# Performance work log

Hardware: AMD Instinct MI355X
Metric: run time of the kernel (lower is better)

The kernel has to match this reference:

```python
import jax, jax.numpy as jnp
import numpy as np

MIN_WEIGHT = 0.1
NEIGH = 2  # consistency_neigh
INV_LOG2 = 1.0 / np.log(2.0)


def _entropy_logits(y):
    # 1 + (p*(y - log(exp(y)+1)) - (1-p)*log(exp(y)+1)) / log(2)
    p = jax.nn.sigmoid(y)
    sp = jax.nn.softplus(y)  # log(exp(y) + 1)
    return 1.0 + (p * (y - sp) - (1.0 - p) * sp) * INV_LOG2


def _consistency(y):
    # 24-offset shifted-neighbor stencil: accumulate squared differences of
    # sigmoid probabilities against each in-bounds neighbor, normalize by the
    # per-pixel valid-neighbor count.
    probas = jax.nn.sigmoid(y)
    _, _, H, W = y.shape
    acc = jnp.zeros_like(y)
    div = jnp.zeros(y.shape, dtype=y.dtype)
    for off_x in range(-NEIGH, NEIGH + 1):
        for off_y in range(-NEIGH, NEIGH + 1):
            if off_x == 0 and off_y == 0:
                continue
            ryl, ryh = max(0, off_y), min(H, H + off_y)
            rxl, rxh = max(0, off_x), min(W, W + off_x)
            tyl, tyh = max(0, -off_y), min(H, H - off_y)
            txl, txh = max(0, -off_x), min(W, W - off_x)
            d = jnp.square(probas[:, :, ryl:ryh, rxl:rxh]
                           - probas[:, :, tyl:tyh, txl:txh])
            acc = acc.at[:, :, ryl:ryh, rxl:rxh].add(d)
            div = div.at[:, :, ryl:ryh, rxl:rxh].add(1.0)
    return 1.0 - acc / div


def setup_inputs() -> dict:
    key = jax.random.key(0)
    k1, k2 = jax.random.split(key)
    y_d = jax.random.normal(k1, (32, 1, 768, 768), dtype=jnp.float32)
    y_gt = jax.random.uniform(k2, (32, 1, 768, 768), dtype=jnp.float32)
    return {"y_d": y_d, "y_gt": y_gt}


def reference(y_d, y_gt):
    # mode = 'pred_merged': consistency * entropy
    w = _consistency(y_d) * _entropy_logits(y_d)
    w = jnp.maximum(w, y_gt)
    w = (1.0 - MIN_WEIGHT) * w + MIN_WEIGHT
    # do_rescale: divide by per-image spatial mean
    w = w / jnp.mean(w, axis=(2, 3), keepdims=True)
    return w
```

## Files before the change

kernel.cpp:

```cpp
#include <hip/hip_runtime.h>

#define IMG_H 768
#define IMG_W 768
#define N_IMG 32
#define TILE 64
#define HALO 2
#define LW 68
#define INV_LOG2 1.44269504088896340736f
#define TILES_X 12
#define TILES_PER_IMG 144
#define NTILES (N_IMG * TILES_PER_IMG)
#define GRID1 1536

__device__ __forceinline__ float fast_sigmoid(float y) {
    return 1.0f / (1.0f + __expf(-y));
}

__global__ __launch_bounds__(256) void wk_pass1(
    const float* __restrict__ y_d, const float* __restrict__ y_gt,
    float* __restrict__ out, float* __restrict__ sums)
{
    __shared__ float pbuf[LW * LW];
    __shared__ float red[4];

    const int tid = threadIdx.x;
    const int c0 = (tid & 15) << 2;
    const int rb = (tid >> 4) << 2;

    for (int it = 0; it < 3; ++it) {
        const int tile = blockIdx.x + it * GRID1;
        const int img = tile / TILES_PER_IMG;
        const int t   = tile - img * TILES_PER_IMG;
        const int ti  = t / TILES_X;
        const int tj  = t - ti * TILES_X;
        const int gi0 = ti * TILE, gj0 = tj * TILE;

        const size_t img_off = (size_t)img * IMG_H * IMG_W;
        const float* __restrict__ yimg = y_d + img_off;
        const float* __restrict__ gimg = y_gt + img_off;
        float* __restrict__ oimg = out + img_off;
        const int gj = gj0 + c0;

        if (it > 0) __syncthreads();

        float4 yv4[4];
#pragma unroll
        for (int r = 0; r < 4; ++r)
            yv4[r] = *reinterpret_cast<const float4*>(
                &yimg[(size_t)(gi0 + rb + r) * IMG_W + gj]);

        float4 pv4[4], ev4[4];
#pragma unroll
        for (int r = 0; r < 4; ++r) {
            float yy[4] = {yv4[r].x, yv4[r].y, yv4[r].z, yv4[r].w};
            float pp[4], ee[4];
#pragma unroll
            for (int u = 0; u < 4; ++u) {
                float y  = yy[u];
                float E  = __expf(-fabsf(y));
                float tt = 1.0f + E;
                float rr = __fdividef(1.0f, tt);
                float p  = (y >= 0.0f) ? rr : E * rr;
                float sp = fmaxf(y, 0.0f) + __logf(tt);
                pp[u] = p;
                ee[u] = fmaf(fmaf(p, y, -sp), INV_LOG2, 1.0f);
            }
            pv4[r] = make_float4(pp[0], pp[1], pp[2], pp[3]);
            ev4[r] = make_float4(ee[0], ee[1], ee[2], ee[3]);
            *reinterpret_cast<float4*>(
                &pbuf[(rb + HALO + r) * LW + (c0 + HALO)]) = pv4[r];
        }

        for (int idx = tid; idx < 528; idx += 256) {
            int pr, pc;
            if (idx < 272) {
                int rsel = idx / 68;
                pr = (rsel < 2) ? rsel : (64 + rsel);
                pc = idx - rsel * 68;
            } else {
                int k = idx - 272;
                pr = (k >> 2) + 2;
                int h = k & 3;
                pc = (h < 2) ? h : (64 + h);
            }
            int gi_ = gi0 - HALO + pr;
            int gj_ = gj0 - HALO + pc;
            float p = 0.f;
            if ((unsigned)gi_ < (unsigned)IMG_H && (unsigned)gj_ < (unsigned)IMG_W)
                p = fast_sigmoid(yimg[(size_t)gi_ * IMG_W + gj_]);
            pbuf[pr * LW + pc] = p;
        }
        __syncthreads();

        float cxv[4], rcp5[4];
#pragma unroll
        for (int c = 0; c < 4; ++c) {
            int g = gj + c;
            cxv[c] = (float)(min(g, HALO) + min(IMG_W - 1 - g, HALO) + 1);
            rcp5[c] = __fdividef(1.0f, fmaf(5.0f, cxv[c], -1.0f));
        }

        float V1[8], V2[8];
#pragma unroll
        for (int cc = 0; cc < 8; ++cc) { V1[cc] = 0.f; V2[cc] = 0.f; }
#pragma unroll
        for (int k = 0; k < 5; ++k) {
            const float* row = &pbuf[(rb + k) * LW + c0];
            float4 A = *reinterpret_cast<const float4*>(row);
            float4 B = *reinterpret_cast<const float4*>(row + 4);
            float a[8] = {A.x, A.y, A.z, A.w, B.x, B.y, B.z, B.w};
#pragma unroll
            for (int cc = 0; cc < 8; ++cc) {
                V1[cc] += a[cc];
                V2[cc] = fmaf(a[cc], a[cc], V2[cc]);
            }
        }

        float lsum = 0.0f;

#pragma unroll
        for (int r = 0; r < 4; ++r) {
            const int gi = gi0 + rb + r;

            float4 g4 = *reinterpret_cast<const float4*>(
                &gimg[(size_t)gi * IMG_W + gj]);

            float t01 = V1[0] + V1[1], t12 = V1[1] + V1[2], t23 = V1[2] + V1[3];
            float t34 = V1[3] + V1[4], t45 = V1[4] + V1[5], t56 = V1[5] + V1[6];
            float S1v[4] = { t01 + t23 + V1[4], t12 + t34 + V1[5],
                             t23 + t45 + V1[6], t34 + t56 + V1[7] };
            float u01 = V2[0] + V2[1], u12 = V2[1] + V2[2], u23 = V2[2] + V2[3];
            float u34 = V2[3] + V2[4], u45 = V2[4] + V2[5], u56 = V2[5] + V2[6];
            float S2v[4] = { u01 + u23 + V2[4], u12 + u34 + V2[5],
                             u23 + u45 + V2[6], u34 + u56 + V2[7] };

            float cy = (float)(min(gi, HALO) + min(IMG_H - 1 - gi, HALO) + 1);
            float rc[4];
            if (cy == 5.0f) {
#pragma unroll
                for (int c = 0; c < 4; ++c) rc[c] = rcp5[c];
            } else {
#pragma unroll
                for (int c = 0; c < 4; ++c)
                    rc[c] = __fdividef(1.0f, fmaf(cy, cxv[c], -1.0f));
            }

            float pcv[4] = {pv4[r].x, pv4[r].y, pv4[r].z, pv4[r].w};
            float ev[4]  = {ev4[r].x, ev4[r].y, ev4[r].z, ev4[r].w};
            float gv[4]  = {g4.x, g4.y, g4.z, g4.w};
            float wv[4];
#pragma unroll
            for (int c = 0; c < 4; ++c) {
                float pc = pcv[c];
                float C = cy * cxv[c];
                float acc = fmaf(C * pc, pc, fmaf(-2.0f * pc, S1v[c], S2v[c]));
                float cons = fmaf(-acc, rc[c], 1.0f);
                float w = fmaxf(cons * ev[c], gv[c]);
                w = fmaf(w, 0.9f, 0.1f);
                wv[c] = w;
                lsum += w;
            }
            *reinterpret_cast<float4*>(&oimg[(size_t)gi * IMG_W + gj]) =
                make_float4(wv[0], wv[1], wv[2], wv[3]);

            if (r < 3) {
                const float* rin  = &pbuf[(rb + r + 5) * LW + c0];
                const float* rout = &pbuf[(rb + r) * LW + c0];
                float4 IA = *reinterpret_cast<const float4*>(rin);
                float4 IB = *reinterpret_cast<const float4*>(rin + 4);
                float4 OA = *reinterpret_cast<const float4*>(rout);
                float4 OB = *reinterpret_cast<const float4*>(rout + 4);
                float vin[8]  = {IA.x, IA.y, IA.z, IA.w, IB.x, IB.y, IB.z, IB.w};
                float vout[8] = {OA.x, OA.y, OA.z, OA.w, OB.x, OB.y, OB.z, OB.w};
#pragma unroll
                for (int cc = 0; cc < 8; ++cc) {
                    V1[cc] += vin[cc] - vout[cc];
                    V2[cc] += fmaf(vin[cc], vin[cc], -(vout[cc] * vout[cc]));
                }
            }
        }

#pragma unroll
        for (int off = 32; off > 0; off >>= 1)
            lsum += __shfl_down(lsum, off, 64);
        if ((tid & 63) == 0) red[tid >> 6] = lsum;
        __syncthreads();
        if (tid == 0)
            atomicAdd(&sums[img], (red[0] + red[1]) + (red[2] + red[3]));
    }
}

__global__ __launch_bounds__(256) void wk_pass2(
    float* __restrict__ out, const float* __restrict__ sums)
{
    const size_t total4 = (size_t)N_IMG * IMG_H * IMG_W / 4;
    const int per_img4 = IMG_H * IMG_W / 4;
    for (size_t i = (size_t)blockIdx.x * blockDim.x + threadIdx.x; i < total4;
         i += (size_t)gridDim.x * blockDim.x) {
        int img = (int)(i / per_img4);
        float scale = (float)(IMG_H * IMG_W) / sums[img];
        float4 v = reinterpret_cast<float4*>(out)[i];
        v.x *= scale; v.y *= scale; v.z *= scale; v.w *= scale;
        reinterpret_cast<float4*>(out)[i] = v;
    }
}

extern "C" void kernel_launch(void* const* d_in, const int* in_sizes, int n_in,
                              void* d_out, int out_size, void* d_ws, size_t ws_size,
                              hipStream_t stream) {
    const float* y_d  = (const float*)d_in[0];
    const float* y_gt = (const float*)d_in[1];
    float* out  = (float*)d_out;
    float* sums = (float*)d_ws;

    hipMemsetAsync(sums, 0, N_IMG * sizeof(float), stream);

    wk_pass1<<<dim3(GRID1), dim3(256), 0, stream>>>(y_d, y_gt, out, sums);
    wk_pass2<<<dim3(2048), dim3(256), 0, stream>>>(out, sums);
}
```

Baseline: 94.75 us.

## Prefetch next tile's logits and issue halo/gt loads before compute

The persistent tile loop now loads the next tile's y_d values into registers during the current iteration. The halo values and the whole 4x4 block of y_gt are read before the sigmoid and entropy math rather than inside the output loop. This is meant to hide global-memory latency behind arithmetic and remove the extra barrier at the top of the loop. In exchange it holds more values in registers, which may lower occupancy.

```diff
diff --git a/kernel.cpp b/kernel.cpp
--- a/kernel.cpp
+++ b/kernel.cpp
@@ -27,69 +27,107 @@
     const int c0 = (tid & 15) << 2;
     const int rb = (tid >> 4) << 2;
 
+    int tile = blockIdx.x;
+    int img = tile / TILES_PER_IMG;
+    int tt  = tile - img * TILES_PER_IMG;
+    int ti  = tt / TILES_X;
+    int tj  = tt - ti * TILES_X;
+    int gi0 = ti * TILE, gj0 = tj * TILE;
+
+    float4 ycur[4];
+    {
+        const float* __restrict__ yimg = y_d + (size_t)img * IMG_H * IMG_W;
+#pragma unroll
+        for (int r = 0; r < 4; ++r)
+            ycur[r] = *reinterpret_cast<const float4*>(
+                &yimg[(size_t)(gi0 + rb + r) * IMG_W + gj0 + c0]);
+    }
+
     for (int it = 0; it < 3; ++it) {
-        const int tile = blockIdx.x + it * GRID1;
-        const int img = tile / TILES_PER_IMG;
-        const int t   = tile - img * TILES_PER_IMG;
-        const int ti  = t / TILES_X;
-        const int tj  = t - ti * TILES_X;
-        const int gi0 = ti * TILE, gj0 = tj * TILE;
-
         const size_t img_off = (size_t)img * IMG_H * IMG_W;
         const float* __restrict__ yimg = y_d + img_off;
         const float* __restrict__ gimg = y_gt + img_off;
         float* __restrict__ oimg = out + img_off;
         const int gj = gj0 + c0;
 
-        if (it > 0) __syncthreads();
-
-        float4 yv4[4];
-#pragma unroll
-        for (int r = 0; r < 4; ++r)
-            yv4[r] = *reinterpret_cast<const float4*>(
-                &yimg[(size_t)(gi0 + rb + r) * IMG_W + gj]);
-
-        float4 pv4[4], ev4[4];
-#pragma unroll
-        for (int r = 0; r < 4; ++r) {
-            float yy[4] = {yv4[r].x, yv4[r].y, yv4[r].z, yv4[r].w};
-            float pp[4], ee[4];
-#pragma unroll
-            for (int u = 0; u < 4; ++u) {
-                float y  = yy[u];
-                float E  = __expf(-fabsf(y));
-                float tt = 1.0f + E;
-                float rr = __fdividef(1.0f, tt);
-                float p  = (y >= 0.0f) ? rr : E * rr;
-                float sp = fmaxf(y, 0.0f) + __logf(tt);
-                pp[u] = p;
-                ee[u] = fmaf(fmaf(p, y, -sp), INV_LOG2, 1.0f);
-            }
-            pv4[r] = make_float4(pp[0], pp[1], pp[2], pp[3]);
-            ev4[r] = make_float4(ee[0], ee[1], ee[2], ee[3]);
-            *reinterpret_cast<float4*>(
-                &pbuf[(rb + HALO + r) * LW + (c0 + HALO)]) = pv4[r];
-        }
-
-        for (int idx = tid; idx < 528; idx += 256) {
+        float hraw[3]; int hpr[3], hpc[3]; bool hact[3], hval[3];
+#pragma unroll
+        for (int k = 0; k < 3; ++k) {
+            int idx = tid + (k << 8);
+            hact[k] = idx < 528;
             int pr, pc;
             if (idx < 272) {
                 int rsel = idx / 68;
                 pr = (rsel < 2) ? rsel : (64 + rsel);
                 pc = idx - rsel * 68;
             } else {
-                int k = idx - 272;
-                pr = (k >> 2) + 2;
-                int h = k & 3;
+                int kk = idx - 272;
+                pr = (kk >> 2) + 2;
+                int h = kk & 3;
                 pc = (h < 2) ? h : (64 + h);
             }
             int gi_ = gi0 - HALO + pr;
             int gj_ = gj0 - HALO + pc;
-            float p = 0.f;
-            if ((unsigned)gi_ < (unsigned)IMG_H && (unsigned)gj_ < (unsigned)IMG_W)
-                p = fast_sigmoid(yimg[(size_t)gi_ * IMG_W + gj_]);
-            pbuf[pr * LW + pc] = p;
-        }
+            hval[k] = hact[k] && (unsigned)gi_ < (unsigned)IMG_H
+                              && (unsigned)gj_ < (unsigned)IMG_W;
+            hraw[k] = hval[k] ? yimg[(size_t)gi_ * IMG_W + gj_] : 0.0f;
+            hpr[k] = pr; hpc[k] = pc;
+        }
+
+        float4 gv4[4];
+#pragma unroll
+        for (int r = 0; r < 4; ++r)
+            gv4[r] = *reinterpret_cast<const float4*>(
+                &gimg[(size_t)(gi0 + rb + r) * IMG_W + gj]);
+
+        float4 pv4[4], ev4[4];
+#pragma unroll
+        for (int r = 0; r < 4; ++r) {
+            float yy[4] = {ycur[r].x, ycur[r].y, ycur[r].z, ycur[r].w};
+            float pp[4], ee[4];
+#pragma unroll
+            for (int u = 0; u < 4; ++u) {
+                float y  = yy[u];
+                float E  = __expf(-fabsf(y));
+                float t2 = 1.0f + E;
+                float rr = __fdividef(1.0f, t2);
+                float p  = (y >= 0.0f) ? rr : E * rr;
+                float sp = fmaxf(y, 0.0f) + __logf(t2);
+                pp[u] = p;
+                ee[u] = fmaf(fmaf(p, y, -sp), INV_LOG2, 1.0f);
+            }
+            pv4[r] = make_float4(pp[0], pp[1], pp[2], pp[3]);
+            ev4[r] = make_float4(ee[0], ee[1], ee[2], ee[3]);
+            *reinterpret_cast<float4*>(
+                &pbuf[(rb + HALO + r) * LW + (c0 + HALO)]) = pv4[r];
+        }
+
+#pragma unroll
+        for (int k = 0; k < 3; ++k) {
+            if (hact[k]) {
+                float p = hval[k] ? fast_sigmoid(hraw[k]) : 0.0f;
+                pbuf[hpr[k] * LW + hpc[k]] = p;
+            }
+        }
+
+        int ntile = tile + GRID1;
+        int nimg = 0, ngi0 = 0, ngj0 = 0;
+        if (it < 2) {
+            nimg = ntile / TILES_PER_IMG;
+            int nt = ntile - nimg * TILES_PER_IMG;
+            int nti = nt / TILES_X;
+            int ntj = nt - nti * TILES_X;
+            ngi0 = nti * TILE; ngj0 = ntj * TILE;
+            const float* __restrict__ yimg2 = y_d + (size_t)nimg * IMG_H * IMG_W;
+            float4 ynxt[4];
+#pragma unroll
+            for (int r = 0; r < 4; ++r)
+                ynxt[r] = *reinterpret_cast<const float4*>(
+                    &yimg2[(size_t)(ngi0 + rb + r) * IMG_W + ngj0 + c0]);
+#pragma unroll
+            for (int r = 0; r < 4; ++r) ycur[r] = ynxt[r];
+        }
+
         __syncthreads();
 
         float cxv[4], rcp5[4];
@@ -121,9 +159,6 @@
 #pragma unroll
         for (int r = 0; r < 4; ++r) {
             const int gi = gi0 + rb + r;
-
-            float4 g4 = *reinterpret_cast<const float4*>(
-                &gimg[(size_t)gi * IMG_W + gj]);
 
             float t01 = V1[0] + V1[1], t12 = V1[1] + V1[2], t23 = V1[2] + V1[3];
             float t34 = V1[3] + V1[4], t45 = V1[4] + V1[5], t56 = V1[5] + V1[6];
@@ -147,7 +182,7 @@
 
             float pcv[4] = {pv4[r].x, pv4[r].y, pv4[r].z, pv4[r].w};
             float ev[4]  = {ev4[r].x, ev4[r].y, ev4[r].z, ev4[r].w};
-            float gv[4]  = {g4.x, g4.y, g4.z, g4.w};
+            float gv[4]  = {gv4[r].x, gv4[r].y, gv4[r].z, gv4[r].w};
             float wv[4];
 #pragma unroll
             for (int c = 0; c < 4; ++c) {
@@ -187,6 +222,8 @@
         __syncthreads();
         if (tid == 0)
             atomicAdd(&sums[img], (red[0] + red[1]) + (red[2] + red[3]));
+
+        tile = ntile; img = nimg; gi0 = ngi0; gj0 = ngj0;
     }
 }
 
```

Result: slower. 97.38 us (+2.8%).

## Use one tile per block and add a specialized interior-tile fast path

Applied to the files above, without the earlier changes.

The pass-1 launch changes from a 1536-block grid looping over three tiles to one block per tile (4608 blocks), which removes the per-iteration barrier and recomputed indexing. Interior tiles get a branch with no bounds checks on halo loads and a constant 1/24 normalizer, while edge tiles keep the general count-based path. Center probabilities are now re-read from shared memory instead of held in registers, and horizontal window sums use a sliding formulation, both to reduce register pressure. The extra code paths enlarge the kernel, and the sliding sums slightly change floating-point rounding.

```diff
diff --git a/kernel.cpp b/kernel.cpp
--- a/kernel.cpp
+++ b/kernel.cpp
@@ -9,12 +9,34 @@
 #define INV_LOG2 1.44269504088896340736f
 #define TILES_X 12
 #define TILES_PER_IMG 144
-#define NTILES (N_IMG * TILES_PER_IMG)
-#define GRID1 1536
 
 __device__ __forceinline__ float fast_sigmoid(float y) {
     return 1.0f / (1.0f + __expf(-y));
 }
+
+#define SLIDE(rr)                                                              \
+    do {                                                                       \
+        const float* rin  = &pbuf[((rr) + 5) * LW + c0];                       \
+        const float* rout = &pbuf[(rr) * LW + c0];                             \
+        float4 IA = *reinterpret_cast<const float4*>(rin);                     \
+        float4 IB = *reinterpret_cast<const float4*>(rin + 4);                 \
+        float4 OA = *reinterpret_cast<const float4*>(rout);                    \
+        float4 OB = *reinterpret_cast<const float4*>(rout + 4);                \
+        float vin[8]  = {IA.x, IA.y, IA.z, IA.w, IB.x, IB.y, IB.z, IB.w};      \
+        float vout[8] = {OA.x, OA.y, OA.z, OA.w, OB.x, OB.y, OB.z, OB.w};      \
+        _Pragma("unroll")                                                      \
+        for (int cc = 0; cc < 8; ++cc) {                                       \
+            V1[cc] += vin[cc] - vout[cc];                                      \
+            V2[cc] += fmaf(vin[cc], vin[cc], -(vout[cc] * vout[cc]));          \
+        }                                                                      \
+    } while (0)
+
+#define HSUMS(S, V)                                                            \
+    float S[4];                                                                \
+    S[0] = ((V[0] + V[1]) + (V[2] + V[3])) + V[4];                             \
+    S[1] = S[0] - V[0] + V[5];                                                 \
+    S[2] = S[1] - V[1] + V[6];                                                 \
+    S[3] = S[2] - V[2] + V[7];
 
 __global__ __launch_bounds__(256) void wk_pass1(
     const float* __restrict__ y_d, const float* __restrict__ y_gt,
@@ -23,138 +45,114 @@
     __shared__ float pbuf[LW * LW];
     __shared__ float red[4];
 
+    const int b = blockIdx.x;
+    const int img = b / TILES_PER_IMG;
+    const int t = b - img * TILES_PER_IMG;
+    const int ti = t / TILES_X;
+    const int tj = t - ti * TILES_X;
+    const int gi0 = ti * TILE, gj0 = tj * TILE;
+    const bool interior = ((unsigned)(ti - 1) < 10u) && ((unsigned)(tj - 1) < 10u);
+
+    const size_t img_off = (size_t)img * IMG_H * IMG_W;
+    const float* __restrict__ yimg = y_d + img_off;
+    const float* __restrict__ gimg = y_gt + img_off;
+    float* __restrict__ oimg = out + img_off;
+
     const int tid = threadIdx.x;
     const int c0 = (tid & 15) << 2;
     const int rb = (tid >> 4) << 2;
-
-    for (int it = 0; it < 3; ++it) {
-        const int tile = blockIdx.x + it * GRID1;
-        const int img = tile / TILES_PER_IMG;
-        const int t   = tile - img * TILES_PER_IMG;
-        const int ti  = t / TILES_X;
-        const int tj  = t - ti * TILES_X;
-        const int gi0 = ti * TILE, gj0 = tj * TILE;
-
-        const size_t img_off = (size_t)img * IMG_H * IMG_W;
-        const float* __restrict__ yimg = y_d + img_off;
-        const float* __restrict__ gimg = y_gt + img_off;
-        float* __restrict__ oimg = out + img_off;
-        const int gj = gj0 + c0;
-
-        if (it > 0) __syncthreads();
-
-        float4 yv4[4];
-#pragma unroll
-        for (int r = 0; r < 4; ++r)
-            yv4[r] = *reinterpret_cast<const float4*>(
-                &yimg[(size_t)(gi0 + rb + r) * IMG_W + gj]);
-
-        float4 pv4[4], ev4[4];
-#pragma unroll
-        for (int r = 0; r < 4; ++r) {
-            float yy[4] = {yv4[r].x, yv4[r].y, yv4[r].z, yv4[r].w};
-            float pp[4], ee[4];
-#pragma unroll
-            for (int u = 0; u < 4; ++u) {
-                float y  = yy[u];
-                float E  = __expf(-fabsf(y));
-                float tt = 1.0f + E;
-                float rr = __fdividef(1.0f, tt);
-                float p  = (y >= 0.0f) ? rr : E * rr;
-                float sp = fmaxf(y, 0.0f) + __logf(tt);
-                pp[u] = p;
-                ee[u] = fmaf(fmaf(p, y, -sp), INV_LOG2, 1.0f);
-            }
-            pv4[r] = make_float4(pp[0], pp[1], pp[2], pp[3]);
-            ev4[r] = make_float4(ee[0], ee[1], ee[2], ee[3]);
-            *reinterpret_cast<float4*>(
-                &pbuf[(rb + HALO + r) * LW + (c0 + HALO)]) = pv4[r];
-        }
-
-        for (int idx = tid; idx < 528; idx += 256) {
-            int pr, pc;
-            if (idx < 272) {
-                int rsel = idx / 68;
-                pr = (rsel < 2) ? rsel : (64 + rsel);
-                pc = idx - rsel * 68;
-            } else {
-                int k = idx - 272;
-                pr = (k >> 2) + 2;
-                int h = k & 3;
-                pc = (h < 2) ? h : (64 + h);
-            }
-            int gi_ = gi0 - HALO + pr;
-            int gj_ = gj0 - HALO + pc;
-            float p = 0.f;
+    const int gj = gj0 + c0;
+
+    float4 ev4[4];
+#pragma unroll
+    for (int r = 0; r < 4; ++r) {
+        float4 y4 = *reinterpret_cast<const float4*>(
+            &yimg[(size_t)(gi0 + rb + r) * IMG_W + gj]);
+        float yy[4] = {y4.x, y4.y, y4.z, y4.w};
+        float pp[4], ee[4];
+#pragma unroll
+        for (int u = 0; u < 4; ++u) {
+            float y  = yy[u];
+            float E  = __expf(-fabsf(y));
+            float t2 = 1.0f + E;
+            float rr = __fdividef(1.0f, t2);
+            float p  = (y >= 0.0f) ? rr : E * rr;
+            float sp = fmaxf(y, 0.0f) + __logf(t2);
+            pp[u] = p;
+            ee[u] = fmaf(fmaf(p, y, -sp), INV_LOG2, 1.0f);
+        }
+        *reinterpret_cast<float4*>(&pbuf[(rb + HALO + r) * LW + (c0 + HALO)]) =
+            make_float4(pp[0], pp[1], pp[2], pp[3]);
+        ev4[r] = make_float4(ee[0], ee[1], ee[2], ee[3]);
+    }
+
+    for (int idx = tid; idx < 528; idx += 256) {
+        int pr, pc;
+        if (idx < 272) {
+            int rsel = idx / 68;
+            pr = (rsel < 2) ? rsel : (64 + rsel);
+            pc = idx - rsel * 68;
+        } else {
+            int k = idx - 272;
+            pr = (k >> 2) + 2;
+            int h = k & 3;
+            pc = (h < 2) ? h : (64 + h);
+        }
+        int gi_ = gi0 - HALO + pr;
+        int gj_ = gj0 - HALO + pc;
+        float p;
+        if (interior) {
+            p = fast_sigmoid(yimg[(size_t)gi_ * IMG_W + gj_]);
+        } else {
+            p = 0.0f;
             if ((unsigned)gi_ < (unsigned)IMG_H && (unsigned)gj_ < (unsigned)IMG_W)
                 p = fast_sigmoid(yimg[(size_t)gi_ * IMG_W + gj_]);
-            pbuf[pr * LW + pc] = p;
-        }
-        __syncthreads();
-
-        float cxv[4], rcp5[4];
-#pragma unroll
-        for (int c = 0; c < 4; ++c) {
-            int g = gj + c;
-            cxv[c] = (float)(min(g, HALO) + min(IMG_W - 1 - g, HALO) + 1);
-            rcp5[c] = __fdividef(1.0f, fmaf(5.0f, cxv[c], -1.0f));
-        }
-
-        float V1[8], V2[8];
-#pragma unroll
-        for (int cc = 0; cc < 8; ++cc) { V1[cc] = 0.f; V2[cc] = 0.f; }
-#pragma unroll
-        for (int k = 0; k < 5; ++k) {
-            const float* row = &pbuf[(rb + k) * LW + c0];
-            float4 A = *reinterpret_cast<const float4*>(row);
-            float4 B = *reinterpret_cast<const float4*>(row + 4);
-            float a[8] = {A.x, A.y, A.z, A.w, B.x, B.y, B.z, B.w};
-#pragma unroll
-            for (int cc = 0; cc < 8; ++cc) {
-                V1[cc] += a[cc];
-                V2[cc] = fmaf(a[cc], a[cc], V2[cc]);
-            }
-        }
-
-        float lsum = 0.0f;
-
+        }
+        pbuf[pr * LW + pc] = p;
+    }
+    __syncthreads();
+
+    float V1[8], V2[8];
+#pragma unroll
+    for (int cc = 0; cc < 8; ++cc) { V1[cc] = 0.f; V2[cc] = 0.f; }
+#pragma unroll
+    for (int k = 0; k < 5; ++k) {
+        const float* row = &pbuf[(rb + k) * LW + c0];
+        float4 A = *reinterpret_cast<const float4*>(row);
+        float4 B = *reinterpret_cast<const float4*>(row + 4);
+        float a[8] = {A.x, A.y, A.z, A.w, B.x, B.y, B.z, B.w};
+#pragma unroll
+        for (int cc = 0; cc < 8; ++cc) {
+            V1[cc] += a[cc];
+            V2[cc] = fmaf(a[cc], a[cc], V2[cc]);
+        }
+    }
+
+    float lsum = 0.0f;
+
+    if (interior) {
+        const float RC = 1.0f / 24.0f;
 #pragma unroll
         for (int r = 0; r < 4; ++r) {
             const int gi = gi0 + rb + r;
-
             float4 g4 = *reinterpret_cast<const float4*>(
                 &gimg[(size_t)gi * IMG_W + gj]);
-
-            float t01 = V1[0] + V1[1], t12 = V1[1] + V1[2], t23 = V1[2] + V1[3];
-            float t34 = V1[3] + V1[4], t45 = V1[4] + V1[5], t56 = V1[5] + V1[6];
-            float S1v[4] = { t01 + t23 + V1[4], t12 + t34 + V1[5],
-                             t23 + t45 + V1[6], t34 + t56 + V1[7] };
-            float u01 = V2[0] + V2[1], u12 = V2[1] + V2[2], u23 = V2[2] + V2[3];
-            float u34 = V2[3] + V2[4], u45 = V2[4] + V2[5], u56 = V2[5] + V2[6];
-            float S2v[4] = { u01 + u23 + V2[4], u12 + u34 + V2[5],
-                             u23 + u45 + V2[6], u34 + u56 + V2[7] };
-
-            float cy = (float)(min(gi, HALO) + min(IMG_H - 1 - gi, HALO) + 1);
-            float rc[4];
-            if (cy == 5.0f) {
-#pragma unroll
-                for (int c = 0; c < 4; ++c) rc[c] = rcp5[c];
-            } else {
-#pragma unroll
-                for (int c = 0; c < 4; ++c)
-                    rc[c] = __fdividef(1.0f, fmaf(cy, cxv[c], -1.0f));
-            }
-
-            float pcv[4] = {pv4[r].x, pv4[r].y, pv4[r].z, pv4[r].w};
-            float ev[4]  = {ev4[r].x, ev4[r].y, ev4[r].z, ev4[r].w};
-            float gv[4]  = {g4.x, g4.y, g4.z, g4.w};
+            const float* crow = &pbuf[(rb + r + 2) * LW + (c0 + 2)];
+            float2 pA = *reinterpret_cast<const float2*>(crow);
+            float2 pB = *reinterpret_cast<const float2*>(crow + 2);
+            float pcv[4] = {pA.x, pA.y, pB.x, pB.y};
+
+            HSUMS(S1v, V1)
+            HSUMS(S2v, V2)
+
+            float ev[4] = {ev4[r].x, ev4[r].y, ev4[r].z, ev4[r].w};
+            float gv[4] = {g4.x, g4.y, g4.z, g4.w};
             float wv[4];
 #pragma unroll
             for (int c = 0; c < 4; ++c) {
                 float pc = pcv[c];
-                float C = cy * cxv[c];
-                float acc = fmaf(C * pc, pc, fmaf(-2.0f * pc, S1v[c], S2v[c]));
-                float cons = fmaf(-acc, rc[c], 1.0f);
+                float acc = fmaf(25.0f * pc, pc, fmaf(-2.0f * pc, S1v[c], S2v[c]));
+                float cons = fmaf(-acc, RC, 1.0f);
                 float w = fmaxf(cons * ev[c], gv[c]);
                 w = fmaf(w, 0.9f, 0.1f);
                 wv[c] = w;
@@ -162,32 +160,57 @@
             }
             *reinterpret_cast<float4*>(&oimg[(size_t)gi * IMG_W + gj]) =
                 make_float4(wv[0], wv[1], wv[2], wv[3]);
-
-            if (r < 3) {
-                const float* rin  = &pbuf[(rb + r + 5) * LW + c0];
-                const float* rout = &pbuf[(rb + r) * LW + c0];
-                float4 IA = *reinterpret_cast<const float4*>(rin);
-                float4 IB = *reinterpret_cast<const float4*>(rin + 4);
-                float4 OA = *reinterpret_cast<const float4*>(rout);
-                float4 OB = *reinterpret_cast<const float4*>(rout + 4);
-                float vin[8]  = {IA.x, IA.y, IA.z, IA.w, IB.x, IB.y, IB.z, IB.w};
-                float vout[8] = {OA.x, OA.y, OA.z, OA.w, OB.x, OB.y, OB.z, OB.w};
-#pragma unroll
-                for (int cc = 0; cc < 8; ++cc) {
-                    V1[cc] += vin[cc] - vout[cc];
-                    V2[cc] += fmaf(vin[cc], vin[cc], -(vout[cc] * vout[cc]));
-                }
+            if (r < 3) SLIDE(rb + r);
+        }
+    } else {
+        float cxv[4];
+#pragma unroll
+        for (int c = 0; c < 4; ++c) {
+            int g = gj + c;
+            cxv[c] = (float)(min(g, HALO) + min(IMG_W - 1 - g, HALO) + 1);
+        }
+#pragma unroll
+        for (int r = 0; r < 4; ++r) {
+            const int gi = gi0 + rb + r;
+            float4 g4 = *reinterpret_cast<const float4*>(
+                &gimg[(size_t)gi * IMG_W + gj]);
+            const float* crow = &pbuf[(rb + r + 2) * LW + (c0 + 2)];
+            float2 pA = *reinterpret_cast<const float2*>(crow);
+            float2 pB = *reinterpret_cast<const float2*>(crow + 2);
+            float pcv[4] = {pA.x, pA.y, pB.x, pB.y};
+
+            HSUMS(S1v, V1)
+            HSUMS(S2v, V2)
+
+            float cy = (float)(min(gi, HALO) + min(IMG_H - 1 - gi, HALO) + 1);
+            float ev[4] = {ev4[r].x, ev4[r].y, ev4[r].z, ev4[r].w};
+            float gv[4] = {g4.x, g4.y, g4.z, g4.w};
+            float wv[4];
+#pragma unroll
+            for (int c = 0; c < 4; ++c) {
+                float pc = pcv[c];
+                float C = cy * cxv[c];
+                float rc = __fdividef(1.0f, C - 1.0f);
+                float acc = fmaf(C * pc, pc, fmaf(-2.0f * pc, S1v[c], S2v[c]));
+                float cons = fmaf(-acc, rc, 1.0f);
+                float w = fmaxf(cons * ev[c], gv[c]);
+                w = fmaf(w, 0.9f, 0.1f);
+                wv[c] = w;
+                lsum += w;
             }
-        }
-
-#pragma unroll
-        for (int off = 32; off > 0; off >>= 1)
-            lsum += __shfl_down(lsum, off, 64);
-        if ((tid & 63) == 0) red[tid >> 6] = lsum;
-        __syncthreads();
-        if (tid == 0)
-            atomicAdd(&sums[img], (red[0] + red[1]) + (red[2] + red[3]));
-    }
+            *reinterpret_cast<float4*>(&oimg[(size_t)gi * IMG_W + gj]) =
+                make_float4(wv[0], wv[1], wv[2], wv[3]);
+            if (r < 3) SLIDE(rb + r);
+        }
+    }
+
+#pragma unroll
+    for (int off = 32; off > 0; off >>= 1)
+        lsum += __shfl_down(lsum, off, 64);
+    if ((tid & 63) == 0) red[tid >> 6] = lsum;
+    __syncthreads();
+    if (tid == 0)
+        atomicAdd(&sums[img], (red[0] + red[1]) + (red[2] + red[3]));
 }
 
 __global__ __launch_bounds__(256) void wk_pass2(
@@ -215,6 +238,6 @@
 
     hipMemsetAsync(sums, 0, N_IMG * sizeof(float), stream);
 
-    wk_pass1<<<dim3(GRID1), dim3(256), 0, stream>>>(y_d, y_gt, out, sums);
+    wk_pass1<<<dim3(N_IMG * TILES_PER_IMG), dim3(256), 0, stream>>>(y_d, y_gt, out, sums);
     wk_pass2<<<dim3(2048), dim3(256), 0, stream>>>(out, sums);
 }
```

New measurement: 101.5 us. +7.2%, slower.
